# Performance work log

Measured on AMD Instinct MI355X. Metric: run time of the kernel, lower is better.

The kernel has to match this reference:

```python
import jax, jax.numpy as jnp
import numpy as np

N = 50000
D_IN = 128
HID = 128
HEADS = 4
PER_HEAD = HID // HEADS
NEG_SLOPE = 0.2


def gatv2_conv(x, src, dst, W_l, W_r, att, bias, H, C, n):
    """PyG GATv2Conv: x [n,F], src/dst [E] (self-loops already appended).
    out[i] = sum_{j->i} softmax_i(att . leaky_relu(Wl x_j + Wr x_i)) * (Wl x_j)
    """
    x_l = (x @ W_l).reshape(n, H, C)  # source-side transform
    x_r = (x @ W_r).reshape(n, H, C)  # destination-side transform
    e = jax.nn.leaky_relu(x_l[src] + x_r[dst], NEG_SLOPE)      # [E,H,C]
    alpha = jnp.einsum('ehc,hc->eh', e, att)                    # [E,H]
    # segment softmax over incoming edges of each destination node
    seg_max = jax.ops.segment_max(alpha, dst, num_segments=n)   # [n,H]
    alpha = jnp.exp(alpha - seg_max[dst])
    denom = jax.ops.segment_sum(alpha, dst, num_segments=n)     # [n,H]
    alpha = alpha / denom[dst]
    msg = x_l[src] * alpha[..., None]                           # [E,H,C]
    out = jax.ops.segment_sum(msg, dst, num_segments=n)         # [n,H,C]
    return out.reshape(n, H * C) + bias


def setup_inputs() -> dict:
    key = jax.random.key(0)
    ks = jax.random.split(key, 10)
    E = 800000
    x = jax.random.normal(ks[0], (N, D_IN), dtype=jnp.float32)
    edge_index = jax.random.randint(ks[1], (2, E), 0, N, dtype=jnp.int64)

    def glorot(k, shape):
        lim = float(np.sqrt(6.0 / (shape[0] + shape[1])))
        return jax.random.uniform(k, shape, jnp.float32, -lim, lim)

    # layer 1: GATv2Conv(D_IN, PER_HEAD, heads=HEADS, concat=True)
    W_l1 = glorot(ks[2], (D_IN, HEADS * PER_HEAD))
    W_r1 = glorot(ks[3], (D_IN, HEADS * PER_HEAD))
    att1 = glorot(ks[4], (HEADS, PER_HEAD))
    b1 = jnp.zeros((HEADS * PER_HEAD,), jnp.float32)
    # layer 2: GATv2Conv(HID, HID, heads=1, concat=True)
    W_l2 = glorot(ks[5], (HID, HID))
    W_r2 = glorot(ks[6], (HID, HID))
    att2 = glorot(ks[7], (1, HID))
    b2 = jnp.zeros((HID,), jnp.float32)
    return {"x": x, "edge_index": edge_index,
            "W_l1": W_l1, "W_r1": W_r1, "att1": att1, "b1": b1,
            "W_l2": W_l2, "W_r2": W_r2, "att2": att2, "b2": b2}


def reference(x, edge_index, W_l1, W_r1, att1, b1, W_l2, W_r2, att2, b2):
    # add self-loops (PyG GATv2Conv default add_self_loops=True)
    loops = jnp.arange(N, dtype=edge_index.dtype)
    src = jnp.concatenate([edge_index[0], loops])
    dst = jnp.concatenate([edge_index[1], loops])
    h = gatv2_conv(x, src, dst, W_l1, W_r1, att1, b1, HEADS, PER_HEAD, N)
    h = jax.nn.relu(h)
    out = gatv2_conv(h, src, dst, W_l2, W_r2, att2, b2, 1, HID, N)
    return out
```

## Files before the change

### kernel.cpp

```cpp
#include <hip/hip_runtime.h>
#include <hip/hip_fp16.h>
#include <math.h>


#define NEG_SLOPE 0.2f
#define CHUNKS 128
#define DCAP 8192

typedef _Float16 half8 __attribute__((ext_vector_type(8)));
typedef _Float16 half2v __attribute__((ext_vector_type(2)));
typedef float floatx4 __attribute__((ext_vector_type(4)));

#if defined(__has_builtin)
#if __has_builtin(__builtin_amdgcn_fdot2)
#define HAVE_FDOT2 1
#endif
#endif

template <int CTRL>
__device__ __forceinline__ float dppmov(float x) {
    int xi = __builtin_bit_cast(int, x);
    int r  = __builtin_amdgcn_update_dpp(0, xi, CTRL, 0xF, 0xF, true);
    return __builtin_bit_cast(float, r);
}
#define DPP_XOR1  0xB1
#define DPP_XOR2  0x4E
#define DPP_HMIRR 0x141
#define DPP_MIRR  0x140


__device__ __forceinline__ void sortA_body(int c, const int* __restrict__ dstA,
                                           int* __restrict__ hist_mat,
                                           int E, int Et, int csz) {
    __shared__ int hist[256];
    int tid = threadIdx.x;
    hist[tid] = 0;
    __syncthreads();
    int start = c * csz, stop = min(Et, start + csz);
    for (int e = start + tid; e < stop; e += 256) {
        int d = (e < E) ? dstA[e] : (e - E);
        atomicAdd(&hist[d >> 8], 1);
    }
    __syncthreads();
    hist_mat[tid * CHUNKS + c] = hist[tid];
}

__device__ __forceinline__ void convert_body(int t,
        const float* __restrict__ Wl1, const float* __restrict__ Wr1,
        const float* __restrict__ Wl2, const float* __restrict__ Wr2,
        const float* __restrict__ att1, const float* __restrict__ att2,
        _Float16* __restrict__ Wt1, _Float16* __restrict__ Wt2,
        _Float16* __restrict__ attH) {
    if (t < 65536) {
        int layer = t >> 15;
        int id = t & 32767;
        int c = id >> 7, k = id & 127;
        const float* Wl = layer ? Wl2 : Wl1;
        const float* Wr = layer ? Wr2 : Wr1;
        _Float16* Wt = layer ? Wt2 : Wt1;
        float v = (c < 128) ? Wl[(size_t)k * 128 + c] : Wr[(size_t)k * 128 + (c - 128)];
        Wt[(size_t)c * 128 + k] = (_Float16)v;
    } else {
        int id = t - 65536;
        if (id < 256) {
            float v = (id < 128) ? att1[id] : att2[id - 128];
            attH[id] = (_Float16)v;
        }
    }
}

__device__ __forceinline__ void scan256_body(const int* __restrict__ hist_mat,
                                             int* __restrict__ offs_flat) {
    __shared__ int wsum[4];
    int t = threadIdx.x;
    int lane = t & 63, w = t >> 6;
    const int4* hp = (const int4*)hist_mat + t * 32;
    int local = 0;
    #pragma unroll 8
    for (int j = 0; j < 32; ++j) {
        int4 v = hp[j];
        local += v.x + v.y + v.z + v.w;
    }
    int x = local;
    #pragma unroll
    for (int off = 1; off < 64; off <<= 1) {
        int y = __shfl_up(x, off, 64);
        if (lane >= off) x += y;
    }
    if (lane == 63) wsum[w] = x;
    __syncthreads();
    int woff = 0;
    for (int i = 0; i < w; ++i) woff += wsum[i];
    int run = woff + x - local;
    int4* op = (int4*)offs_flat + t * 32;
    #pragma unroll 8
    for (int j = 0; j < 32; ++j) {
        int4 v = hp[j];
        int4 o;
        o.x = run;
        o.y = run + v.x;
        o.z = o.y + v.y;
        o.w = o.z + v.z;
        run = o.w + v.w;
        op[j] = o;
    }
}

__device__ __forceinline__ void sortC_body(int c, const int* __restrict__ srcA,
        const int* __restrict__ dstA, const int* __restrict__ offs_flat,
        int* __restrict__ packed, int E, int Et, int csz) {
    __shared__ int pos[256];
    int tid = threadIdx.x;
    pos[tid] = offs_flat[tid * CHUNKS + c];
    __syncthreads();
    int start = c * csz, stop = min(Et, start + csz);
    for (int e = start + tid; e < stop; e += 256) {
        int s, d;
        if (e < E) { s = srcA[e]; d = dstA[e]; } else { s = e - E; d = s; }
        int p = atomicAdd(&pos[d >> 8], 1);
        packed[p] = ((d & 255) << 16) | s;
    }
}

#define BPAD 136

template <bool AF32>
__device__ __forceinline__ void gemm_body(int bid, const void* __restrict__ Av,
        const _Float16* __restrict__ Bt, _Float16* __restrict__ outL,
        _Float16* __restrict__ outR, int n) {
    __shared__ _Float16 sB[256 * BPAD];
    int tid = threadIdx.x;
    {
        int c0 = (tid & 15) * 8;
        int r0 = tid >> 4;
        #pragma unroll
        for (int i = 0; i < 16; ++i) {
            int r = r0 + i * 16;
            *(half8*)(sB + r * BPAD + c0) = *(const half8*)(Bt + (size_t)r * 128 + c0);
        }
    }
    int wave = tid >> 6;
    int lane = tid & 63;
    int ln = lane & 15;
    int q  = lane >> 4;
    int row0 = bid * 64 + wave * 16;

    int arow = row0 + ln;
    if (arow >= n) arow = n - 1;
    half8 a0, a1, a2, a3;
    if (AF32) {
        const float* ap = (const float*)Av + (size_t)arow * 128 + q * 8;
        #pragma unroll
        for (int g = 0; g < 4; ++g) {
            float4 f0 = *(const float4*)(ap + g * 32);
            float4 f1 = *(const float4*)(ap + g * 32 + 4);
            half8 h;
            h[0] = (_Float16)f0.x; h[1] = (_Float16)f0.y;
            h[2] = (_Float16)f0.z; h[3] = (_Float16)f0.w;
            h[4] = (_Float16)f1.x; h[5] = (_Float16)f1.y;
            h[6] = (_Float16)f1.z; h[7] = (_Float16)f1.w;
            if (g == 0) a0 = h; else if (g == 1) a1 = h;
            else if (g == 2) a2 = h; else a3 = h;
        }
    } else {
        const _Float16* ap = (const _Float16*)Av + (size_t)arow * 128 + q * 8;
        a0 = *(const half8*)(ap);
        a1 = *(const half8*)(ap + 32);
        a2 = *(const half8*)(ap + 64);
        a3 = *(const half8*)(ap + 96);
    }

    __syncthreads();

    floatx4 acc[16];
    #pragma unroll
    for (int ct = 0; ct < 16; ++ct) {
        const _Float16* bp = sB + (ct * 16 + ln) * BPAD + q * 8;
        half8 b0 = *(const half8*)(bp);
        half8 b1 = *(const half8*)(bp + 32);
        half8 b2 = *(const half8*)(bp + 64);
        half8 b3 = *(const half8*)(bp + 96);
        floatx4 c = {0.f, 0.f, 0.f, 0.f};
        c = __builtin_amdgcn_mfma_f32_16x16x32_f16(a0, b0, c, 0, 0, 0);
        c = __builtin_amdgcn_mfma_f32_16x16x32_f16(a1, b1, c, 0, 0, 0);
        c = __builtin_amdgcn_mfma_f32_16x16x32_f16(a2, b2, c, 0, 0, 0);
        c = __builtin_amdgcn_mfma_f32_16x16x32_f16(a3, b3, c, 0, 0, 0);
        acc[ct] = c;
    }

    #pragma unroll
    for (int ct = 0; ct < 16; ++ct) {
        int col = ct * 16 + ln;
        #pragma unroll
        for (int r = 0; r < 4; ++r) {
            int grow = row0 + q * 4 + r;
            if (grow < n) {
                _Float16 v = (_Float16)acc[ct][r];
                if (ct < 8) outL[(size_t)grow * 128 + col] = v;
                else        outR[(size_t)grow * 128 + (col - 128)] = v;
            }
        }
    }
}


__global__ __launch_bounds__(256)
void fused_pre(const int* __restrict__ dstA, int* __restrict__ hist_mat,
               int E, int Et, int csz,
               const float* __restrict__ Wl1, const float* __restrict__ Wr1,
               const float* __restrict__ Wl2, const float* __restrict__ Wr2,
               const float* __restrict__ att1, const float* __restrict__ att2,
               _Float16* __restrict__ Wt1, _Float16* __restrict__ Wt2,
               _Float16* __restrict__ attH) {
    if (blockIdx.x < CHUNKS) {
        sortA_body(blockIdx.x, dstA, hist_mat, E, Et, csz);
    } else {
        int t = (blockIdx.x - CHUNKS) * 256 + threadIdx.x;
        convert_body(t, Wl1, Wr1, Wl2, Wr2, att1, att2, Wt1, Wt2, attH);
    }
}

__global__ __launch_bounds__(256)
void fused_scan_gemm(const int* __restrict__ hist_mat, int* __restrict__ offs_flat,
                     const float* __restrict__ X, const _Float16* __restrict__ Wt1,
                     _Float16* __restrict__ outL, _Float16* __restrict__ outR, int n) {
    if (blockIdx.x == 0) {
        scan256_body(hist_mat, offs_flat);
    } else {
        gemm_body<true>(blockIdx.x - 1, X, Wt1, outL, outR, n);
    }
}

__global__ __launch_bounds__(256)
void fused_mid(const int* __restrict__ srcA, const int* __restrict__ dstA,
               const int* __restrict__ offs_flat, int* __restrict__ packed,
               int E, int Et, int csz, int gemm_base,
               const float* __restrict__ X, const _Float16* __restrict__ Wt1,
               _Float16* __restrict__ outL, _Float16* __restrict__ outR, int n) {
    if (blockIdx.x < CHUNKS) {
        sortC_body(blockIdx.x, srcA, dstA, offs_flat, packed, E, Et, csz);
    } else {
        gemm_body<true>(blockIdx.x - CHUNKS + gemm_base, X, Wt1, outL, outR, n);
    }
}

__global__ __launch_bounds__(256)
void gemm_l2(const _Float16* __restrict__ A, const _Float16* __restrict__ Bt,
             _Float16* __restrict__ outL, _Float16* __restrict__ outR, int n) {
    gemm_body<false>(blockIdx.x, A, Bt, outL, outR, n);
}

__global__ __launch_bounds__(256)
void sortD_fine(const int* __restrict__ offs_flat, const int* __restrict__ packed,
                int* __restrict__ rowptr, int* __restrict__ srcs,
                int n, int Et, int nbuck) {
    __shared__ int stage[DCAP];
    __shared__ int sorted[DCAP];
    __shared__ int hist[256], curv[256], wsumD[4];
    int tid = threadIdx.x, b = blockIdx.x;
    int base = offs_flat[b * CHUNKS];
    int end  = (b == nbuck - 1) ? Et : offs_flat[(b + 1) * CHUNKS];
    int m = min(end - base, DCAP);

    hist[tid] = 0;
    for (int i = tid; i < m; i += 256) stage[i] = packed[base + i];
    __syncthreads();
    for (int i = tid; i < m; i += 256) atomicAdd(&hist[stage[i] >> 16], 1);
    __syncthreads();
    {
        int v = hist[tid];
        int lane = tid & 63, w = tid >> 6;
        int x = v;
        #pragma unroll
        for (int off = 1; off < 64; off <<= 1) {
            int y = __shfl_up(x, off, 64);
            if (lane >= off) x += y;
        }
        if (lane == 63) wsumD[w] = x;
        __syncthreads();
        int woff = 0;
        for (int i = 0; i < w; ++i) woff += wsumD[i];
        int excl = woff + x - v;
        curv[tid] = excl;
        int node0 = b << 8;
        if (node0 + tid < n) rowptr[node0 + tid] = base + excl;
        if (b == 0 && tid == 0) rowptr[n] = Et;
    }
    __syncthreads();
    for (int i = tid; i < m; i += 256) {
        int p = stage[i];
        int pos = atomicAdd(&curv[p >> 16], 1);
        sorted[pos] = p & 0xFFFF;
    }
    __syncthreads();
    for (int i = tid; i < m; i += 256) srcs[base + i] = sorted[i];
}


template <bool LAYER1>
__global__ __launch_bounds__(256)
void edge_aggregate(const _Float16* __restrict__ xl, const _Float16* __restrict__ xr,
                    const _Float16* __restrict__ attH, const float* __restrict__ bias,
                    const int* __restrict__ rowptr, const int* __restrict__ srcs,
                    void* __restrict__ outv, int n) {
    int node = blockIdx.x * (blockDim.x >> 6) + (threadIdx.x >> 6);
    int lane = threadIdx.x & 63;
    if (node >= n) return;
    int ln = lane & 15;
    int q  = lane >> 4;
    int c0 = ln * 8;

    half8 xrh = *(const half8*)(xr + (size_t)node * 128 + c0);
    half8 ahh = *(const half8*)(attH + c0);

    float acc[8] = {0.f, 0.f, 0.f, 0.f, 0.f, 0.f, 0.f, 0.f};
    float l = 0.f;

    auto proc = [&](half8 vh, bool valid) {
        half8 e  = vh + xrh;
        half8 es = e * (_Float16)NEG_SLOPE;
        half8 lr = __builtin_elementwise_max(e, es);
        float p = 0.f;
        #pragma unroll
        for (int k = 0; k < 4; ++k) {
            half2v ee = { lr[2 * k], lr[2 * k + 1] };
            half2v aa = { ahh[2 * k], ahh[2 * k + 1] };
#ifdef HAVE_FDOT2
            p = __builtin_amdgcn_fdot2(ee, aa, p, false);
#else
            p = fmaf((float)ee[0], (float)aa[0], p);
            p = fmaf((float)ee[1], (float)aa[1], p);
#endif
        }
        p += dppmov<DPP_XOR1>(p);
        p += dppmov<DPP_XOR2>(p);
        if (!LAYER1) { p += dppmov<DPP_HMIRR>(p); p += dppmov<DPP_MIRR>(p); }
        float pe = __expf(p);
        if (!valid) pe = 0.f;
        l += pe;
        #pragma unroll
        for (int k = 0; k < 8; ++k) acc[k] = fmaf(pe, (float)vh[k], acc[k]);
    };

    int jb = rowptr[node], je = rowptr[node + 1];
    for (int base = jb; base < je; base += 64) {
        int idx = base + lane;
        int myS = (idx < je) ? srcs[idx] : 0;
        int cnt = min(64, je - base);
        int t = 0;
        for (; t + 16 <= cnt; t += 16) {
            int s0 = __shfl(myS, t + q, 64);
            int s1 = __shfl(myS, t + 4 + q, 64);
            int s2 = __shfl(myS, t + 8 + q, 64);
            int s3 = __shfl(myS, t + 12 + q, 64);
            half8 v0 = *(const half8*)(xl + (size_t)s0 * 128 + c0);
            half8 v1 = *(const half8*)(xl + (size_t)s1 * 128 + c0);
            half8 v2 = *(const half8*)(xl + (size_t)s2 * 128 + c0);
            half8 v3 = *(const half8*)(xl + (size_t)s3 * 128 + c0);
            proc(v0, true); proc(v1, true); proc(v2, true); proc(v3, true);
        }
        for (; t < cnt; t += 4) {
            int sa = __shfl(myS, t + q, 64);
            half8 va = *(const half8*)(xl + (size_t)sa * 128 + c0);
            proc(va, (t + q) < cnt);
        }
    }

    #pragma unroll
    for (int k = 0; k < 8; ++k) {
        acc[k] += __shfl_xor(acc[k], 16, 64);
        acc[k] += __shfl_xor(acc[k], 32, 64);
    }
    l += __shfl_xor(l, 16, 64);
    l += __shfl_xor(l, 32, 64);

    float inv = 1.0f / l;
    float bv[8];
    *(float4*)&bv[0] = *(const float4*)(bias + c0);
    *(float4*)&bv[4] = *(const float4*)(bias + c0 + 4);
    float o[8];
    #pragma unroll
    for (int k = 0; k < 8; ++k) {
        o[k] = acc[k] * inv + bv[k];
        if (LAYER1) o[k] = fmaxf(o[k], 0.f);
    }
    if (lane < 16) {
        if (LAYER1) {
            __half2 hh2[4];
            #pragma unroll
            for (int k = 0; k < 4; ++k) hh2[k] = __floats2half2_rn(o[2 * k], o[2 * k + 1]);
            *(float4*)((_Float16*)outv + (size_t)node * 128 + c0) = *(float4*)&hh2[0];
        } else {
            float* out = (float*)outv;
            *(float4*)(out + (size_t)node * 128 + c0)     = *(float4*)&o[0];
            *(float4*)(out + (size_t)node * 128 + c0 + 4) = *(float4*)&o[4];
        }
    }
}


extern "C" void kernel_launch(void* const* d_in, const int* in_sizes, int n_in,
                              void* d_out, int out_size, void* d_ws, size_t ws_size,
                              hipStream_t stream) {
    const float* x    = (const float*)d_in[0];
    const int*   ei   = (const int*)d_in[1];
    const float* Wl1  = (const float*)d_in[2];
    const float* Wr1  = (const float*)d_in[3];
    const float* att1 = (const float*)d_in[4];
    const float* b1   = (const float*)d_in[5];
    const float* Wl2  = (const float*)d_in[6];
    const float* Wr2  = (const float*)d_in[7];
    const float* att2 = (const float*)d_in[8];
    const float* b2   = (const float*)d_in[9];

    int n  = in_sizes[0] / 128;
    int E  = in_sizes[1] / 2;
    int Et = E + n;

    _Float16* xlh  = (_Float16*)d_ws;
    _Float16* xrh2 = xlh + (size_t)n * 128;
    _Float16* hh   = xrh2 + (size_t)n * 128;
    _Float16* Wt1  = hh  + (size_t)n * 128;
    _Float16* Wt2  = Wt1 + 256 * 128;
    _Float16* attH = Wt2 + 256 * 128;
    int* rowptr   = (int*)(attH + 256);
    int* srcs     = rowptr + ((n + 4) & ~3);
    int* packed   = srcs + Et;
    int* hist_mat = packed + Et;
    int* offs_flat= hist_mat + CHUNKS * 256;

    const int* srcA = ei;
    const int* dstA = ei + E;

    int csz   = (Et + CHUNKS - 1) / CHUNKS;
    int nbuck = (n + 255) >> 8;
    int gemm_grid = (n + 63) / 64;
    int edge_grid = (n + 3) / 4;
    int GA = gemm_grid >> 1;
    int GB = gemm_grid - GA;

    fused_pre<<<CHUNKS + 257, 256, 0, stream>>>(
        dstA, hist_mat, E, Et, csz,
        Wl1, Wr1, Wl2, Wr2, att1, att2, Wt1, Wt2, attH);
    fused_scan_gemm<<<1 + GA, 256, 0, stream>>>(
        hist_mat, offs_flat, x, Wt1, xlh, xrh2, n);
    fused_mid<<<CHUNKS + GB, 256, 0, stream>>>(
        srcA, dstA, offs_flat, packed, E, Et, csz, GA,
        x, Wt1, xlh, xrh2, n);
    sortD_fine<<<nbuck, 256, 0, stream>>>(offs_flat, packed, rowptr, srcs, n, Et, nbuck);
    edge_aggregate<true><<<edge_grid, 256, 0, stream>>>(
        xlh, xrh2, attH, b1, rowptr, srcs, hh, n);
    gemm_l2<<<gemm_grid, 256, 0, stream>>>(hh, Wt2, xlh, xrh2, n);
    edge_aggregate<false><<<edge_grid, 256, 0, stream>>>(
        xlh, xrh2, attH + 128, b2, rowptr, srcs, d_out, n);
}
```

Measured before the change: 217.4 us.

## Map one 16-lane group per destination node in edge aggregation

The edge aggregation kernel now assigns 16 lanes per destination node instead of a full 64-lane wavefront, so each wave processes four nodes. Each group walks its neighbor list four edges at a time, loading source indices directly from memory. This removes the shuffle-based index broadcast and the cross-quarter reductions, and cuts wasted lanes for nodes of average degree around 17. In exchange, each group handles its edges serially, and nodes of different degree within a wave can diverge.

```diff
diff --git a/kernel.cpp b/kernel.cpp
--- a/kernel.cpp
+++ b/kernel.cpp
@@ -303,11 +303,9 @@
                     const _Float16* __restrict__ attH, const float* __restrict__ bias,
                     const int* __restrict__ rowptr, const int* __restrict__ srcs,
                     void* __restrict__ outv, int n) {
-    int node = blockIdx.x * (blockDim.x >> 6) + (threadIdx.x >> 6);
-    int lane = threadIdx.x & 63;
+    int node = blockIdx.x * (blockDim.x >> 4) + (threadIdx.x >> 4);
+    int ln = threadIdx.x & 15;
     if (node >= n) return;
-    int ln = lane & 15;
-    int q  = lane >> 4;
     int c0 = ln * 8;
 
     half8 xrh = *(const half8*)(xr + (size_t)node * 128 + c0);
@@ -343,36 +341,20 @@
     };
 
     int jb = rowptr[node], je = rowptr[node + 1];
-    for (int base = jb; base < je; base += 64) {
-        int idx = base + lane;
-        int myS = (idx < je) ? srcs[idx] : 0;
-        int cnt = min(64, je - base);
-        int t = 0;
-        for (; t + 16 <= cnt; t += 16) {
-            int s0 = __shfl(myS, t + q, 64);
-            int s1 = __shfl(myS, t + 4 + q, 64);
-            int s2 = __shfl(myS, t + 8 + q, 64);
-            int s3 = __shfl(myS, t + 12 + q, 64);
-            half8 v0 = *(const half8*)(xl + (size_t)s0 * 128 + c0);
-            half8 v1 = *(const half8*)(xl + (size_t)s1 * 128 + c0);
-            half8 v2 = *(const half8*)(xl + (size_t)s2 * 128 + c0);
-            half8 v3 = *(const half8*)(xl + (size_t)s3 * 128 + c0);
-            proc(v0, true); proc(v1, true); proc(v2, true); proc(v3, true);
-        }
-        for (; t < cnt; t += 4) {
-            int sa = __shfl(myS, t + q, 64);
-            half8 va = *(const half8*)(xl + (size_t)sa * 128 + c0);
-            proc(va, (t + q) < cnt);
-        }
-    }
-
-    #pragma unroll
-    for (int k = 0; k < 8; ++k) {
-        acc[k] += __shfl_xor(acc[k], 16, 64);
-        acc[k] += __shfl_xor(acc[k], 32, 64);
-    }
-    l += __shfl_xor(l, 16, 64);
-    l += __shfl_xor(l, 32, 64);
+    for (int t = jb; t < je; t += 4) {
+        int s0 = srcs[t];
+        int s1 = (t + 1 < je) ? srcs[t + 1] : s0;
+        int s2 = (t + 2 < je) ? srcs[t + 2] : s0;
+        int s3 = (t + 3 < je) ? srcs[t + 3] : s0;
+        half8 v0 = *(const half8*)(xl + (size_t)s0 * 128 + c0);
+        half8 v1 = *(const half8*)(xl + (size_t)s1 * 128 + c0);
+        half8 v2 = *(const half8*)(xl + (size_t)s2 * 128 + c0);
+        half8 v3 = *(const half8*)(xl + (size_t)s3 * 128 + c0);
+        proc(v0, true);
+        proc(v1, t + 1 < je);
+        proc(v2, t + 2 < je);
+        proc(v3, t + 3 < je);
+    }
 
     float inv = 1.0f / l;
     float bv[8];
@@ -384,17 +366,15 @@
         o[k] = acc[k] * inv + bv[k];
         if (LAYER1) o[k] = fmaxf(o[k], 0.f);
     }
-    if (lane < 16) {
-        if (LAYER1) {
-            __half2 hh2[4];
-            #pragma unroll
-            for (int k = 0; k < 4; ++k) hh2[k] = __floats2half2_rn(o[2 * k], o[2 * k + 1]);
-            *(float4*)((_Float16*)outv + (size_t)node * 128 + c0) = *(float4*)&hh2[0];
-        } else {
-            float* out = (float*)outv;
-            *(float4*)(out + (size_t)node * 128 + c0)     = *(float4*)&o[0];
-            *(float4*)(out + (size_t)node * 128 + c0 + 4) = *(float4*)&o[4];
-        }
+    if (LAYER1) {
+        __half2 hh2[4];
+        #pragma unroll
+        for (int k = 0; k < 4; ++k) hh2[k] = __floats2half2_rn(o[2 * k], o[2 * k + 1]);
+        *(float4*)((_Float16*)outv + (size_t)node * 128 + c0) = *(float4*)&hh2[0];
+    } else {
+        float* out = (float*)outv;
+        *(float4*)(out + (size_t)node * 128 + c0)     = *(float4*)&o[0];
+        *(float4*)(out + (size_t)node * 128 + c0 + 4) = *(float4*)&o[4];
     }
 }
 
@@ -435,7 +415,7 @@
     int csz   = (Et + CHUNKS - 1) / CHUNKS;
     int nbuck = (n + 255) >> 8;
     int gemm_grid = (n + 63) / 64;
-    int edge_grid = (n + 3) / 4;
+    int edge_grid = (n + 15) / 16;
     int GA = gemm_grid >> 1;
     int GB = gemm_grid - GA;
 
```

New measurement: 227.4 us. 1.05x slower.

## Overlap layer-2 GEMM with second half of layer-1 aggregation; use exp2

Applied to the files above, without the earlier changes.

Layer-1 aggregation is split into two halves. The second half runs in the same launch as the layer-2 GEMM on the first half of rows, and a final GEMM launch covers the remaining rows. Layer-2 projections now go to separate xl2/xr2 buffers so the GEMM cannot overwrite layer-1 features that are still being read. Attention weights are pre-scaled by log2(e) so the softmax can use the native exp2 instruction instead of __expf. The cost is one extra launch and more workspace, and the fp16 pre-scaling adds a small rounding difference.

```diff
diff --git a/kernel.cpp b/kernel.cpp
--- a/kernel.cpp
+++ b/kernel.cpp
@@ -15,7 +15,16 @@
 #if __has_builtin(__builtin_amdgcn_fdot2)
 #define HAVE_FDOT2 1
 #endif
+#if __has_builtin(__builtin_amdgcn_exp2f)
+#define EXP2F(x) __builtin_amdgcn_exp2f(x)
+#else
+#define EXP2F(x) exp2f(x)
 #endif
+#else
+#define EXP2F(x) exp2f(x)
+#endif
+
+#define LOG2E 1.44269504f
 
 template <int CTRL>
 __device__ __forceinline__ float dppmov(float x) {
@@ -64,7 +73,7 @@
         int id = t - 65536;
         if (id < 256) {
             float v = (id < 128) ? att1[id] : att2[id - 128];
-            attH[id] = (_Float16)v;
+            attH[id] = (_Float16)(v * LOG2E);
         }
     }
 }
@@ -203,107 +212,62 @@
     }
 }
 
-
-__global__ __launch_bounds__(256)
-void fused_pre(const int* __restrict__ dstA, int* __restrict__ hist_mat,
-               int E, int Et, int csz,
-               const float* __restrict__ Wl1, const float* __restrict__ Wr1,
-               const float* __restrict__ Wl2, const float* __restrict__ Wr2,
-               const float* __restrict__ att1, const float* __restrict__ att2,
-               _Float16* __restrict__ Wt1, _Float16* __restrict__ Wt2,
-               _Float16* __restrict__ attH) {
-    if (blockIdx.x < CHUNKS) {
-        sortA_body(blockIdx.x, dstA, hist_mat, E, Et, csz);
-    } else {
-        int t = (blockIdx.x - CHUNKS) * 256 + threadIdx.x;
-        convert_body(t, Wl1, Wr1, Wl2, Wr2, att1, att2, Wt1, Wt2, attH);
-    }
-}
-
-__global__ __launch_bounds__(256)
-void fused_scan_gemm(const int* __restrict__ hist_mat, int* __restrict__ offs_flat,
-                     const float* __restrict__ X, const _Float16* __restrict__ Wt1,
-                     _Float16* __restrict__ outL, _Float16* __restrict__ outR, int n) {
-    if (blockIdx.x == 0) {
-        scan256_body(hist_mat, offs_flat);
-    } else {
-        gemm_body<true>(blockIdx.x - 1, X, Wt1, outL, outR, n);
-    }
-}
-
-__global__ __launch_bounds__(256)
-void fused_mid(const int* __restrict__ srcA, const int* __restrict__ dstA,
-               const int* __restrict__ offs_flat, int* __restrict__ packed,
-               int E, int Et, int csz, int gemm_base,
-               const float* __restrict__ X, const _Float16* __restrict__ Wt1,
-               _Float16* __restrict__ outL, _Float16* __restrict__ outR, int n) {
-    if (blockIdx.x < CHUNKS) {
-        sortC_body(blockIdx.x, srcA, dstA, offs_flat, packed, E, Et, csz);
-    } else {
-        gemm_body<true>(blockIdx.x - CHUNKS + gemm_base, X, Wt1, outL, outR, n);
-    }
-}
-
-__global__ __launch_bounds__(256)
-void gemm_l2(const _Float16* __restrict__ A, const _Float16* __restrict__ Bt,
-             _Float16* __restrict__ outL, _Float16* __restrict__ outR, int n) {
-    gemm_body<false>(blockIdx.x, A, Bt, outL, outR, n);
-}
-
-__global__ __launch_bounds__(256)
-void sortD_fine(const int* __restrict__ offs_flat, const int* __restrict__ packed,
-                int* __restrict__ rowptr, int* __restrict__ srcs,
-                int n, int Et, int nbuck) {
-    __shared__ int stage[DCAP];
-    __shared__ int sorted[DCAP];
-    __shared__ int hist[256], curv[256], wsumD[4];
-    int tid = threadIdx.x, b = blockIdx.x;
-    int base = offs_flat[b * CHUNKS];
-    int end  = (b == nbuck - 1) ? Et : offs_flat[(b + 1) * CHUNKS];
-    int m = min(end - base, DCAP);
-
-    hist[tid] = 0;
-    for (int i = tid; i < m; i += 256) stage[i] = packed[base + i];
-    __syncthreads();
-    for (int i = tid; i < m; i += 256) atomicAdd(&hist[stage[i] >> 16], 1);
-    __syncthreads();
-    {
-        int v = hist[tid];
-        int lane = tid & 63, w = tid >> 6;
-        int x = v;
-        #pragma unroll
-        for (int off = 1; off < 64; off <<= 1) {
-            int y = __shfl_up(x, off, 64);
-            if (lane >= off) x += y;
-        }
-        if (lane == 63) wsumD[w] = x;
-        __syncthreads();
-        int woff = 0;
-        for (int i = 0; i < w; ++i) woff += wsumD[i];
-        int excl = woff + x - v;
-        curv[tid] = excl;
-        int node0 = b << 8;
-        if (node0 + tid < n) rowptr[node0 + tid] = base + excl;
-        if (b == 0 && tid == 0) rowptr[n] = Et;
-    }
-    __syncthreads();
-    for (int i = tid; i < m; i += 256) {
-        int p = stage[i];
-        int pos = atomicAdd(&curv[p >> 16], 1);
-        sorted[pos] = p & 0xFFFF;
-    }
-    __syncthreads();
-    for (int i = tid; i < m; i += 256) srcs[base + i] = sorted[i];
+__device__ __forceinline__ void gemm_noB_body(int bid, const _Float16* __restrict__ A,
+        const _Float16* __restrict__ Bt, _Float16* __restrict__ outL,
+        _Float16* __restrict__ outR, int n) {
+    int tid = threadIdx.x;
+    int wave = tid >> 6;
+    int lane = tid & 63;
+    int ln = lane & 15;
+    int q  = lane >> 4;
+    int row0 = bid * 64 + wave * 16;
+
+    int arow = row0 + ln;
+    if (arow >= n) arow = n - 1;
+    const _Float16* ap = A + (size_t)arow * 128 + q * 8;
+    half8 a0 = *(const half8*)(ap);
+    half8 a1 = *(const half8*)(ap + 32);
+    half8 a2 = *(const half8*)(ap + 64);
+    half8 a3 = *(const half8*)(ap + 96);
+
+    floatx4 acc[16];
+    #pragma unroll
+    for (int ct = 0; ct < 16; ++ct) {
+        const _Float16* bp = Bt + (size_t)(ct * 16 + ln) * 128 + q * 8;
+        half8 b0 = *(const half8*)(bp);
+        half8 b1 = *(const half8*)(bp + 32);
+        half8 b2 = *(const half8*)(bp + 64);
+        half8 b3 = *(const half8*)(bp + 96);
+        floatx4 c = {0.f, 0.f, 0.f, 0.f};
+        c = __builtin_amdgcn_mfma_f32_16x16x32_f16(a0, b0, c, 0, 0, 0);
+        c = __builtin_amdgcn_mfma_f32_16x16x32_f16(a1, b1, c, 0, 0, 0);
+        c = __builtin_amdgcn_mfma_f32_16x16x32_f16(a2, b2, c, 0, 0, 0);
+        c = __builtin_amdgcn_mfma_f32_16x16x32_f16(a3, b3, c, 0, 0, 0);
+        acc[ct] = c;
+    }
+
+    #pragma unroll
+    for (int ct = 0; ct < 16; ++ct) {
+        int col = ct * 16 + ln;
+        #pragma unroll
+        for (int r = 0; r < 4; ++r) {
+            int grow = row0 + q * 4 + r;
+            if (grow < n) {
+                _Float16 v = (_Float16)acc[ct][r];
+                if (ct < 8) outL[(size_t)grow * 128 + col] = v;
+                else        outR[(size_t)grow * 128 + (col - 128)] = v;
+            }
+        }
+    }
 }
 
 
 template <bool LAYER1>
-__global__ __launch_bounds__(256)
-void edge_aggregate(const _Float16* __restrict__ xl, const _Float16* __restrict__ xr,
-                    const _Float16* __restrict__ attH, const float* __restrict__ bias,
-                    const int* __restrict__ rowptr, const int* __restrict__ srcs,
-                    void* __restrict__ outv, int n) {
-    int node = blockIdx.x * (blockDim.x >> 6) + (threadIdx.x >> 6);
+__device__ __forceinline__ void agg_body(int node,
+        const _Float16* __restrict__ xl, const _Float16* __restrict__ xr,
+        const _Float16* __restrict__ attH, const float* __restrict__ bias,
+        const int* __restrict__ rowptr, const int* __restrict__ srcs,
+        void* __restrict__ outv, int n) {
     int lane = threadIdx.x & 63;
     if (node >= n) return;
     int ln = lane & 15;
@@ -335,7 +299,7 @@
         p += dppmov<DPP_XOR1>(p);
         p += dppmov<DPP_XOR2>(p);
         if (!LAYER1) { p += dppmov<DPP_HMIRR>(p); p += dppmov<DPP_MIRR>(p); }
-        float pe = __expf(p);
+        float pe = EXP2F(p);
         if (!valid) pe = 0.f;
         l += pe;
         #pragma unroll
@@ -399,6 +363,133 @@
 }
 
 
+__global__ __launch_bounds__(256)
+void fused_pre(const int* __restrict__ dstA, int* __restrict__ hist_mat,
+               int E, int Et, int csz,
+               const float* __restrict__ Wl1, const float* __restrict__ Wr1,
+               const float* __restrict__ Wl2, const float* __restrict__ Wr2,
+               const float* __restrict__ att1, const float* __restrict__ att2,
+               _Float16* __restrict__ Wt1, _Float16* __restrict__ Wt2,
+               _Float16* __restrict__ attH) {
+    if (blockIdx.x < CHUNKS) {
+        sortA_body(blockIdx.x, dstA, hist_mat, E, Et, csz);
+    } else {
+        int t = (blockIdx.x - CHUNKS) * 256 + threadIdx.x;
+        convert_body(t, Wl1, Wr1, Wl2, Wr2, att1, att2, Wt1, Wt2, attH);
+    }
+}
+
+__global__ __launch_bounds__(256)
+void fused_scan_gemm(const int* __restrict__ hist_mat, int* __restrict__ offs_flat,
+                     const float* __restrict__ X, const _Float16* __restrict__ Wt1,
+                     _Float16* __restrict__ outL, _Float16* __restrict__ outR, int n) {
+    if (blockIdx.x == 0) {
+        scan256_body(hist_mat, offs_flat);
+    } else {
+        gemm_body<true>(blockIdx.x - 1, X, Wt1, outL, outR, n);
+    }
+}
+
+__global__ __launch_bounds__(256)
+void fused_mid(const int* __restrict__ srcA, const int* __restrict__ dstA,
+               const int* __restrict__ offs_flat, int* __restrict__ packed,
+               int E, int Et, int csz, int gemm_base,
+               const float* __restrict__ X, const _Float16* __restrict__ Wt1,
+               _Float16* __restrict__ outL, _Float16* __restrict__ outR, int n) {
+    if (blockIdx.x < CHUNKS) {
+        sortC_body(blockIdx.x, srcA, dstA, offs_flat, packed, E, Et, csz);
+    } else {
+        gemm_body<true>(blockIdx.x - CHUNKS + gemm_base, X, Wt1, outL, outR, n);
+    }
+}
+
+__global__ __launch_bounds__(256)
+void agg1_kernel(const _Float16* __restrict__ xl, const _Float16* __restrict__ xr,
+                 const _Float16* __restrict__ attH, const float* __restrict__ bias,
+                 const int* __restrict__ rowptr, const int* __restrict__ srcs,
+                 _Float16* __restrict__ out, int n) {
+    int node = blockIdx.x * 4 + (threadIdx.x >> 6);
+    agg_body<true>(node, xl, xr, attH, bias, rowptr, srcs, out, n);
+}
+
+__global__ __launch_bounds__(256)
+void fused_agg1_gemm2(const _Float16* __restrict__ xl, const _Float16* __restrict__ xr,
+                      const _Float16* __restrict__ attH, const float* __restrict__ bias,
+                      const int* __restrict__ rowptr, const int* __restrict__ srcs,
+                      _Float16* __restrict__ hh, int node_base, int g2, int n,
+                      const _Float16* __restrict__ Wt2,
+                      _Float16* __restrict__ outL2, _Float16* __restrict__ outR2) {
+    if (blockIdx.x < (unsigned)g2) {
+        gemm_noB_body(blockIdx.x, hh, Wt2, outL2, outR2, n);
+    } else {
+        int node = node_base + (blockIdx.x - g2) * 4 + (threadIdx.x >> 6);
+        agg_body<true>(node, xl, xr, attH, bias, rowptr, srcs, hh, n);
+    }
+}
+
+__global__ __launch_bounds__(256)
+void gemm_l2(const _Float16* __restrict__ A, const _Float16* __restrict__ Bt,
+             _Float16* __restrict__ outL, _Float16* __restrict__ outR,
+             int n, int base) {
+    gemm_body<false>(blockIdx.x + base, A, Bt, outL, outR, n);
+}
+
+__global__ __launch_bounds__(256)
+void agg2_kernel(const _Float16* __restrict__ xl, const _Float16* __restrict__ xr,
+                 const _Float16* __restrict__ attH, const float* __restrict__ bias,
+                 const int* __restrict__ rowptr, const int* __restrict__ srcs,
+                 float* __restrict__ out, int n) {
+    int node = blockIdx.x * 4 + (threadIdx.x >> 6);
+    agg_body<false>(node, xl, xr, attH, bias, rowptr, srcs, out, n);
+}
+
+__global__ __launch_bounds__(256)
+void sortD_fine(const int* __restrict__ offs_flat, const int* __restrict__ packed,
+                int* __restrict__ rowptr, int* __restrict__ srcs,
+                int n, int Et, int nbuck) {
+    __shared__ int stage[DCAP];
+    __shared__ int sorted[DCAP];
+    __shared__ int hist[256], curv[256], wsumD[4];
+    int tid = threadIdx.x, b = blockIdx.x;
+    int base = offs_flat[b * CHUNKS];
+    int end  = (b == nbuck - 1) ? Et : offs_flat[(b + 1) * CHUNKS];
+    int m = min(end - base, DCAP);
+
+    hist[tid] = 0;
+    for (int i = tid; i < m; i += 256) stage[i] = packed[base + i];
+    __syncthreads();
+    for (int i = tid; i < m; i += 256) atomicAdd(&hist[stage[i] >> 16], 1);
+    __syncthreads();
+    {
+        int v = hist[tid];
+        int lane = tid & 63, w = tid >> 6;
+        int x = v;
+        #pragma unroll
+        for (int off = 1; off < 64; off <<= 1) {
+            int y = __shfl_up(x, off, 64);
+            if (lane >= off) x += y;
+        }
+        if (lane == 63) wsumD[w] = x;
+        __syncthreads();
+        int woff = 0;
+        for (int i = 0; i < w; ++i) woff += wsumD[i];
+        int excl = woff + x - v;
+        curv[tid] = excl;
+        int node0 = b << 8;
+        if (node0 + tid < n) rowptr[node0 + tid] = base + excl;
+        if (b == 0 && tid == 0) rowptr[n] = Et;
+    }
+    __syncthreads();
+    for (int i = tid; i < m; i += 256) {
+        int p = stage[i];
+        int pos = atomicAdd(&curv[p >> 16], 1);
+        sorted[pos] = p & 0xFFFF;
+    }
+    __syncthreads();
+    for (int i = tid; i < m; i += 256) srcs[base + i] = sorted[i];
+}
+
+
 extern "C" void kernel_launch(void* const* d_in, const int* in_sizes, int n_in,
                               void* d_out, int out_size, void* d_ws, size_t ws_size,
                               hipStream_t stream) {
@@ -428,6 +519,8 @@
     int* packed   = srcs + Et;
     int* hist_mat = packed + Et;
     int* offs_flat= hist_mat + CHUNKS * 256;
+    _Float16* xl2 = (_Float16*)(offs_flat + CHUNKS * 256);
+    _Float16* xr2 = xl2 + (size_t)n * 128;
 
     const int* srcA = ei;
     const int* dstA = ei + E;
@@ -438,6 +531,13 @@
     int edge_grid = (n + 3) / 4;
     int GA = gemm_grid >> 1;
     int GB = gemm_grid - GA;
+
+    int nh   = ((n / 2) + 63) & ~63;
+    if (nh > n) nh = n & ~63;
+    int g2a  = nh >> 6;
+    int g2b  = gemm_grid - g2a;
+    int aggA = nh >> 2;
+    int aggB = (n - nh + 3) >> 2;
 
     fused_pre<<<CHUNKS + 257, 256, 0, stream>>>(
         dstA, hist_mat, E, Et, csz,
@@ -448,9 +548,11 @@
         srcA, dstA, offs_flat, packed, E, Et, csz, GA,
         x, Wt1, xlh, xrh2, n);
     sortD_fine<<<nbuck, 256, 0, stream>>>(offs_flat, packed, rowptr, srcs, n, Et, nbuck);
-    edge_aggregate<true><<<edge_grid, 256, 0, stream>>>(
+    agg1_kernel<<<aggA, 256, 0, stream>>>(
         xlh, xrh2, attH, b1, rowptr, srcs, hh, n);
-    gemm_l2<<<gemm_grid, 256, 0, stream>>>(hh, Wt2, xlh, xrh2, n);
-    edge_aggregate<false><<<edge_grid, 256, 0, stream>>>(
-        xlh, xrh2, attH + 128, b2, rowptr, srcs, d_out, n);
-}
+    fused_agg1_gemm2<<<g2a + aggB, 256, 0, stream>>>(
+        xlh, xrh2, attH, b1, rowptr, srcs, hh, nh, g2a, n, Wt2, xl2, xr2);
+    gemm_l2<<<g2b, 256, 0, stream>>>(hh, Wt2, xl2, xr2, n, g2a);
+    agg2_kernel<<<edge_grid, 256, 0, stream>>>(
+        xl2, xr2, attH + 128, b2, rowptr, srcs, (float*)d_out, n);
+}
```

Result: slower. 246.7 us (+13.5%).

## Process several nodes per wavefront with prefetched edge lists and exp2 softmax

Applied to the files above, without the earlier changes.

Each wavefront in the edge aggregation kernel now handles four consecutive destination nodes instead of one. It loads all their row pointers at once and prefetches the next node's source indices while the current node is processed, which is meant to hide rowptr/srcs load latency and amortise per-wave setup. The attention vectors are pre-scaled by log2(e) so the softmax can use the hardware exp2 instruction instead of __expf. The grid shrinks by four, which reduces the number of waves available for latency hiding and may cause load imbalance from variable node degree.

```diff
diff --git a/kernel.cpp b/kernel.cpp
--- a/kernel.cpp
+++ b/kernel.cpp
@@ -15,7 +15,16 @@
 #if __has_builtin(__builtin_amdgcn_fdot2)
 #define HAVE_FDOT2 1
 #endif
+#if __has_builtin(__builtin_amdgcn_exp2f)
+#define EXP2F(x) __builtin_amdgcn_exp2f(x)
+#else
+#define EXP2F(x) exp2f(x)
 #endif
+#else
+#define EXP2F(x) exp2f(x)
+#endif
+
+#define LOG2E 1.44269504f
 
 template <int CTRL>
 __device__ __forceinline__ float dppmov(float x) {
@@ -64,7 +73,7 @@
         int id = t - 65536;
         if (id < 256) {
             float v = (id < 128) ? att1[id] : att2[id - 128];
-            attH[id] = (_Float16)v;
+            attH[id] = (_Float16)(v * LOG2E);
         }
     }
 }
@@ -297,103 +306,138 @@
 }
 
 
+#define NPW 4
+
 template <bool LAYER1>
 __global__ __launch_bounds__(256)
 void edge_aggregate(const _Float16* __restrict__ xl, const _Float16* __restrict__ xr,
                     const _Float16* __restrict__ attH, const float* __restrict__ bias,
                     const int* __restrict__ rowptr, const int* __restrict__ srcs,
                     void* __restrict__ outv, int n) {
-    int node = blockIdx.x * (blockDim.x >> 6) + (threadIdx.x >> 6);
+    int wid  = blockIdx.x * (blockDim.x >> 6) + (threadIdx.x >> 6);
+    int base = wid * NPW;
+    if (base >= n) return;
     int lane = threadIdx.x & 63;
-    if (node >= n) return;
     int ln = lane & 15;
     int q  = lane >> 4;
     int c0 = ln * 8;
 
-    half8 xrh = *(const half8*)(xr + (size_t)node * 128 + c0);
     half8 ahh = *(const half8*)(attH + c0);
-
-    float acc[8] = {0.f, 0.f, 0.f, 0.f, 0.f, 0.f, 0.f, 0.f};
-    float l = 0.f;
-
-    auto proc = [&](half8 vh, bool valid) {
-        half8 e  = vh + xrh;
-        half8 es = e * (_Float16)NEG_SLOPE;
-        half8 lr = __builtin_elementwise_max(e, es);
-        float p = 0.f;
-        #pragma unroll
-        for (int k = 0; k < 4; ++k) {
-            half2v ee = { lr[2 * k], lr[2 * k + 1] };
-            half2v aa = { ahh[2 * k], ahh[2 * k + 1] };
-#ifdef HAVE_FDOT2
-            p = __builtin_amdgcn_fdot2(ee, aa, p, false);
-#else
-            p = fmaf((float)ee[0], (float)aa[0], p);
-            p = fmaf((float)ee[1], (float)aa[1], p);
-#endif
-        }
-        p += dppmov<DPP_XOR1>(p);
-        p += dppmov<DPP_XOR2>(p);
-        if (!LAYER1) { p += dppmov<DPP_HMIRR>(p); p += dppmov<DPP_MIRR>(p); }
-        float pe = __expf(p);
-        if (!valid) pe = 0.f;
-        l += pe;
-        #pragma unroll
-        for (int k = 0; k < 8; ++k) acc[k] = fmaf(pe, (float)vh[k], acc[k]);
-    };
-
-    int jb = rowptr[node], je = rowptr[node + 1];
-    for (int base = jb; base < je; base += 64) {
-        int idx = base + lane;
-        int myS = (idx < je) ? srcs[idx] : 0;
-        int cnt = min(64, je - base);
-        int t = 0;
-        for (; t + 16 <= cnt; t += 16) {
-            int s0 = __shfl(myS, t + q, 64);
-            int s1 = __shfl(myS, t + 4 + q, 64);
-            int s2 = __shfl(myS, t + 8 + q, 64);
-            int s3 = __shfl(myS, t + 12 + q, 64);
-            half8 v0 = *(const half8*)(xl + (size_t)s0 * 128 + c0);
-            half8 v1 = *(const half8*)(xl + (size_t)s1 * 128 + c0);
-            half8 v2 = *(const half8*)(xl + (size_t)s2 * 128 + c0);
-            half8 v3 = *(const half8*)(xl + (size_t)s3 * 128 + c0);
-            proc(v0, true); proc(v1, true); proc(v2, true); proc(v3, true);
-        }
-        for (; t < cnt; t += 4) {
-            int sa = __shfl(myS, t + q, 64);
-            half8 va = *(const half8*)(xl + (size_t)sa * 128 + c0);
-            proc(va, (t + q) < cnt);
-        }
-    }
-
-    #pragma unroll
-    for (int k = 0; k < 8; ++k) {
-        acc[k] += __shfl_xor(acc[k], 16, 64);
-        acc[k] += __shfl_xor(acc[k], 32, 64);
-    }
-    l += __shfl_xor(l, 16, 64);
-    l += __shfl_xor(l, 32, 64);
-
-    float inv = 1.0f / l;
     float bv[8];
     *(float4*)&bv[0] = *(const float4*)(bias + c0);
     *(float4*)&bv[4] = *(const float4*)(bias + c0 + 4);
-    float o[8];
-    #pragma unroll
-    for (int k = 0; k < 8; ++k) {
-        o[k] = acc[k] * inv + bv[k];
-        if (LAYER1) o[k] = fmaxf(o[k], 0.f);
-    }
-    if (lane < 16) {
-        if (LAYER1) {
-            __half2 hh2[4];
+
+    int rp = 0;
+    if (lane <= NPW) {
+        int idx = base + lane;
+        rp = rowptr[idx < n ? idx : n];
+    }
+
+    int jb_n = __shfl(rp, 0);
+    int je_n = __shfl(rp, 1);
+    int myS_n = 0;
+    {
+        int idx = jb_n + lane;
+        if (idx < je_n) myS_n = srcs[idx];
+    }
+
+    for (int k = 0; k < NPW; ++k) {
+        int node = base + k;
+        if (node >= n) break;
+        int jb = jb_n, je = je_n;
+        int myS0 = myS_n;
+
+        if (k + 1 < NPW && node + 1 < n) {
+            jb_n = __shfl(rp, k + 1);
+            je_n = __shfl(rp, k + 2);
+            int idx = jb_n + lane;
+            myS_n = (idx < je_n) ? srcs[idx] : 0;
+        }
+
+        half8 xrh = *(const half8*)(xr + (size_t)node * 128 + c0);
+        float acc[8] = {0.f, 0.f, 0.f, 0.f, 0.f, 0.f, 0.f, 0.f};
+        float l = 0.f;
+
+        auto proc = [&](half8 vh, bool valid) {
+            half8 e  = vh + xrh;
+            half8 es = e * (_Float16)NEG_SLOPE;
+            half8 lr = __builtin_elementwise_max(e, es);
+            float p = 0.f;
             #pragma unroll
-            for (int k = 0; k < 4; ++k) hh2[k] = __floats2half2_rn(o[2 * k], o[2 * k + 1]);
-            *(float4*)((_Float16*)outv + (size_t)node * 128 + c0) = *(float4*)&hh2[0];
-        } else {
-            float* out = (float*)outv;
-            *(float4*)(out + (size_t)node * 128 + c0)     = *(float4*)&o[0];
-            *(float4*)(out + (size_t)node * 128 + c0 + 4) = *(float4*)&o[4];
+            for (int kk = 0; kk < 4; ++kk) {
+                half2v ee = { lr[2 * kk], lr[2 * kk + 1] };
+                half2v aa = { ahh[2 * kk], ahh[2 * kk + 1] };
+#ifdef HAVE_FDOT2
+                p = __builtin_amdgcn_fdot2(ee, aa, p, false);
+#else
+                p = fmaf((float)ee[0], (float)aa[0], p);
+                p = fmaf((float)ee[1], (float)aa[1], p);
+#endif
+            }
+            p += dppmov<DPP_XOR1>(p);
+            p += dppmov<DPP_XOR2>(p);
+            if (!LAYER1) { p += dppmov<DPP_HMIRR>(p); p += dppmov<DPP_MIRR>(p); }
+            float pe = EXP2F(p);
+            if (!valid) pe = 0.f;
+            l += pe;
+            #pragma unroll
+            for (int kk = 0; kk < 8; ++kk) acc[kk] = fmaf(pe, (float)vh[kk], acc[kk]);
+        };
+
+        for (int b0 = jb; b0 < je; b0 += 64) {
+            int myS;
+            if (b0 == jb) {
+                myS = myS0;
+            } else {
+                int idx = b0 + lane;
+                myS = (idx < je) ? srcs[idx] : 0;
+            }
+            int cnt = min(64, je - b0);
+            int t = 0;
+            for (; t + 16 <= cnt; t += 16) {
+                int s0 = __shfl(myS, t + q, 64);
+                int s1 = __shfl(myS, t + 4 + q, 64);
+                int s2 = __shfl(myS, t + 8 + q, 64);
+                int s3 = __shfl(myS, t + 12 + q, 64);
+                half8 v0 = *(const half8*)(xl + (size_t)s0 * 128 + c0);
+                half8 v1 = *(const half8*)(xl + (size_t)s1 * 128 + c0);
+                half8 v2 = *(const half8*)(xl + (size_t)s2 * 128 + c0);
+                half8 v3 = *(const half8*)(xl + (size_t)s3 * 128 + c0);
+                proc(v0, true); proc(v1, true); proc(v2, true); proc(v3, true);
+            }
+            for (; t < cnt; t += 4) {
+                int sa = __shfl(myS, t + q, 64);
+                half8 va = *(const half8*)(xl + (size_t)sa * 128 + c0);
+                proc(va, (t + q) < cnt);
+            }
+        }
+
+        #pragma unroll
+        for (int kk = 0; kk < 8; ++kk) {
+            acc[kk] += __shfl_xor(acc[kk], 16, 64);
+            acc[kk] += __shfl_xor(acc[kk], 32, 64);
+        }
+        l += __shfl_xor(l, 16, 64);
+        l += __shfl_xor(l, 32, 64);
+
+        float inv = 1.0f / l;
+        float o[8];
+        #pragma unroll
+        for (int kk = 0; kk < 8; ++kk) {
+            o[kk] = acc[kk] * inv + bv[kk];
+            if (LAYER1) o[kk] = fmaxf(o[kk], 0.f);
+        }
+        if (lane < 16) {
+            if (LAYER1) {
+                __half2 hh2[4];
+                #pragma unroll
+                for (int kk = 0; kk < 4; ++kk) hh2[kk] = __floats2half2_rn(o[2 * kk], o[2 * kk + 1]);
+                *(float4*)((_Float16*)outv + (size_t)node * 128 + c0) = *(float4*)&hh2[0];
+            } else {
+                float* out = (float*)outv;
+                *(float4*)(out + (size_t)node * 128 + c0)     = *(float4*)&o[0];
+                *(float4*)(out + (size_t)node * 128 + c0 + 4) = *(float4*)&o[4];
+            }
         }
     }
 }
@@ -435,7 +479,7 @@
     int csz   = (Et + CHUNKS - 1) / CHUNKS;
     int nbuck = (n + 255) >> 8;
     int gemm_grid = (n + 63) / 64;
-    int edge_grid = (n + 3) / 4;
+    int edge_grid = (n + NPW * 4 - 1) / (NPW * 4);
     int GA = gemm_grid >> 1;
     int GB = gemm_grid - GA;
 
```

Result: slower. 225.8 us (+3.8%).
